# Performance work log

Measured on AMD Instinct MI355X. Metric: run time of the kernel, lower is better.

## Reference

```python
import jax, jax.numpy as jnp
import numpy as np

B, T, M, E, H = 8, 1024, 8192, 1024, 128
DECAY = 0.01
LQ_ADD = 1e-4
POS_TABLE_SIZE = 32


def setup_inputs() -> dict:
    key = jax.random.key(0)
    ks = jax.random.split(key, 9)
    return {
        "block_pos_list": jax.random.randint(ks[0], (B,), 0, 10),
        "inp": jax.random.normal(ks[1], (B, T, E), jnp.float32),
        "memory": jax.random.normal(ks[2], (B, M, E), jnp.float32),
        "memory_block_dist": jax.random.randint(ks[3], (B, M), 0, 1000).astype(jnp.int32),
        "memory_rank": jax.random.normal(ks[4], (B, M), jnp.float32),
        "pos_table": jax.random.normal(ks[5], (POS_TABLE_SIZE, E), jnp.float32) * 0.02,
        "Wk": jax.random.normal(ks[6], (H, E), jnp.float32) / np.float32(np.sqrt(E)),
        "Wq": jax.random.normal(ks[7], (H, E), jnp.float32) / np.float32(np.sqrt(E)),
        "Wv": jax.random.normal(ks[8], (H, E), jnp.float32) / np.float32(np.sqrt(E)),
    }


def reference(block_pos_list, inp, memory, memory_block_dist, memory_rank, pos_table, Wk, Wq, Wv):
    # --- reset slots where block_pos == 0 (start of a new work) ---
    reset = (block_pos_list == 0)                               # [B]
    memory = jnp.where(reset[:, None, None], 0.0, memory)       # [B, M, E]
    dist = jnp.where(reset[:, None], 0, memory_block_dist) + 1  # [B, M]

    # --- log2-bucketed positional embedding added to memory ---
    m_pos_ix = jnp.floor(jnp.log2(dist.astype(jnp.float32))).astype(jnp.int32)
    m_with_emb = memory + pos_table[m_pos_ix]                   # [B, M, E]
    mk = jnp.concatenate([m_with_emb, inp], axis=1)             # [B, M+T, E]

    # --- projections (torch Linear: x @ W.T) ---
    k = jnp.einsum('bse,he->bsh', mk, Wk)                       # [B, M+T, H]
    q = jnp.einsum('bte,he->bth', inp, Wq)                      # [B, T, H]
    v = jnp.einsum('bse,he->bsh', mk, Wv)                       # [B, M+T, H]

    # --- square + max-normalize attention (not softmax) ---
    mbs = M + T
    wei = jnp.einsum('bth,bsh->bts', q, k) * np.float32(mbs ** -0.5)  # [B, T, M+T]
    wei = wei * wei
    wei = wei / jnp.max(wei, axis=2, keepdims=True)

    # --- per-slot rank update ---
    mean_wei = jnp.mean(jnp.sum(wei, axis=1), axis=1)           # [B]
    new_rank = memory_rank + jnp.sum(wei[:, :, :M], axis=1) / mean_wei[:, None] - 1.0 - DECAY

    # --- sort memory slots by rank (descending), evict bottom block ---
    order = jnp.argsort(-new_rank, axis=1)                      # [B, M]
    mem_s = jnp.take_along_axis(memory, order[:, :, None], axis=1)
    dist_s = jnp.take_along_axis(dist, order, axis=1)
    rank_s = jnp.take_along_axis(new_rank, order, axis=1)
    r = min(T, M)
    new_memory = jax.lax.stop_gradient(mem_s.at[:, -r:].set(inp[:, -r:]))
    new_dist = dist_s.at[:, -r:].set(0)
    new_rank_out = jax.lax.stop_gradient(rank_s.at[:, -r:].set(1.0))

    qt_loss = jnp.sum(jnp.log(wei + LQ_ADD))
    out = jnp.einsum('bts,bsh->bth', wei, v)                    # [B, T, H]
    return out, qt_loss, new_memory, new_dist, new_rank_out
```

## Files before the change

kernel.cpp:

```cpp
#include <hip/hip_runtime.h>
#include <hip/hip_bf16.h>
#include <stdint.h>

#define BB 8
#define TT 1024
#define MM 8192
#define EE 1024
#define HH 128
#define SS (MM + TT)
#define RKEEP (MM - 1024)
#define NSPLIT 8
#define SCHUNK (SS / NSPLIT)
#define NT (SCHUNK / 64)
#define BK 32

typedef __attribute__((ext_vector_type(8))) short bf16x8;
typedef __attribute__((ext_vector_type(4))) short s16x4;
typedef __attribute__((ext_vector_type(4))) float f32x4;

#define VMCNT(n) asm volatile("s_waitcnt vmcnt(" #n ")" ::: "memory")
#define LGKM0()  asm volatile("s_waitcnt lgkmcnt(0)" ::: "memory")
#define SBAR()   __builtin_amdgcn_s_barrier()
#define SCB()    __builtin_amdgcn_sched_barrier(0)

static __device__ __forceinline__ unsigned f2ord(float f) {
    unsigned u = __float_as_uint(f);
    return u ^ ((u & 0x80000000u) ? 0xFFFFFFFFu : 0x80000000u);
}
static __device__ __forceinline__ float ord2f(unsigned o) {
    unsigned u = (o & 0x80000000u) ? (o ^ 0x80000000u) : ~o;
    return __uint_as_float(u);
}
static __device__ __forceinline__ unsigned short f2bf(float x) {
    unsigned u = __float_as_uint(x);
    unsigned r = u + 0x7FFFu + ((u >> 16) & 1u);
    return (unsigned short)(r >> 16);
}

static __device__ __forceinline__ void gload_lds16(const short* g, short* l) {
    __builtin_amdgcn_global_load_lds(
        (const __attribute__((address_space(1))) void*)g,
        (__attribute__((address_space(3))) void*)l, 16, 0, 0);
}

__device__ const float SCALEF = (float)(1.0 / 96.0);

__global__ __launch_bounds__(256) void k_wsplit(
    const float* __restrict__ Wk, const float* __restrict__ Wq, const float* __restrict__ Wv,
    short* __restrict__ wk, short* __restrict__ wq, short* __restrict__ wv)
{
    int idx = blockIdx.x * 256 + threadIdx.x;
    int m = idx >> 15;
    int o4 = (idx & 32767) * 4;
    const float* W = m == 0 ? Wk : (m == 1 ? Wq : Wv);
    short* D = m == 0 ? wk : (m == 1 ? wq : wv);
    f32x4 v = *(const f32x4*)&W[o4];
    s16x4 h;
#pragma unroll
    for (int j = 0; j < 4; ++j) h[j] = (short)f2bf(v[j]);
    *(s16x4*)&D[o4] = h;
}

__global__ __launch_bounds__(256, 2) void k_proj_kv(
    const float* __restrict__ memory, const int* __restrict__ mbd,
    const int* __restrict__ bpl, const float* __restrict__ pos_table,
    const float* __restrict__ inp,
    const short* __restrict__ wk, const short* __restrict__ wv,
    short* __restrict__ kb, short* __restrict__ vT)
{
    __shared__ __align__(16) short smA[2][64 * 64];
    __shared__ __align__(16) short smB[3][2][128 * 32];

    const int tid = threadIdx.x;
    const int b   = blockIdx.y;
    const int s0  = blockIdx.x * 64;
    const bool reset = (bpl[b] == 0);
    const int lane = tid & 63, wid = tid >> 6;
    const int wc = wid;
    const int fr = lane & 15, fq = lane >> 4;

    const int arow = tid >> 2;
    const int aq   = tid & 3;
    int pix;
    const float* abase;
    {
        int s = s0 + arow;
        if (s < MM) {
            int d = reset ? 1 : (mbd[b * MM + s] + 1);
            pix = 31 - __clz(d);
            abase = reset ? nullptr : &memory[((size_t)b * MM + s) * EE];
        } else {
            pix = -1;
            abase = &inp[((size_t)b * TT + (s - MM)) * EE];
        }
    }

    f32x4 accK[4][2], accV[4][2];
#pragma unroll
    for (int m = 0; m < 4; ++m)
#pragma unroll
        for (int n = 0; n < 2; ++n) {
            accK[m][n] = (f32x4){0.f, 0.f, 0.f, 0.f};
            accV[m][n] = (f32x4){0.f, 0.f, 0.f, 0.f};
        }

    const int wh   = (tid >> 2);
    const int wk8  = (tid & 3) * 8;
    const int wdst = wid * 512;

    auto STAGEW = [&](int e0, int buf) {
#pragma unroll
        for (int p = 0; p < 2; ++p) {
            int h = p * 64 + wh;
            int ec = wk8 ^ ((h & 3) << 3);
            size_t g = (size_t)h * EE + e0 + ec;
            gload_lds16(&wk[g], &smB[buf][0][p * 2048 + wdst]);
            gload_lds16(&wv[g], &smB[buf][1][p * 2048 + wdst]);
        }
    };
    auto LOADP = [&](int p, f32x4 xa[4]) {
        int e0 = p * 64 + aq * 16;
#pragma unroll
        for (int j = 0; j < 4; ++j) {
            f32x4 v = (f32x4){0.f, 0.f, 0.f, 0.f};
            if (abase) v = *(const f32x4*)&abase[e0 + j * 4];
            if (pix >= 0) {
                f32x4 pt = *(const f32x4*)&pos_table[(size_t)pix * EE + e0 + j * 4];
                v[0] += pt[0]; v[1] += pt[1]; v[2] += pt[2]; v[3] += pt[3];
            }
            xa[j] = v;
        }
    };
    auto STOREP = [&](const f32x4 xa[4], int abuf) {
#pragma unroll
        for (int j = 0; j < 2; ++j) {
            bf16x8 h;
#pragma unroll
            for (int c = 0; c < 4; ++c) {
                h[c]     = (short)f2bf(xa[2 * j][c]);
                h[4 + c] = (short)f2bf(xa[2 * j + 1][c]);
            }
            int g = (aq * 2 + j) ^ (arow & 7);
            *(bf16x8*)&smA[abuf][arow * 64 + g * 8] = h;
        }
    };

    f32x4 xa[4];
    LOADP(0, xa);
    STOREP(xa, 0);
    STAGEW(0, 0);
    STAGEW(BK, 1);
    __syncthreads();
    LOADP(1, xa);

    for (int step = 0; step < 32; ++step) {
        if (step == 31)                        { VMCNT(0); }
        else if ((step & 1) || step == 30)     { VMCNT(4); }
        else                                   { VMCNT(8); }
        SBAR(); SCB();
        if (step <= 29) STAGEW((step + 2) * BK, (step + 2) % 3);

        const int wbuf = step % 3;
        const int pbuf = (step >> 1) & 1;
        bf16x8 ah[4];
#pragma unroll
        for (int m = 0; m < 4; ++m) {
            int r = m * 16 + fr;
            int g = (((step & 1) * 4) + fq) ^ (r & 7);
            ah[m] = *(const bf16x8*)&smA[pbuf][r * 64 + g * 8];
        }
#pragma unroll
        for (int n = 0; n < 2; ++n) {
            int c = wc * 32 + n * 16 + fr;
            int off = c * 32 + ((fq * 8) ^ ((c & 3) << 3));
            bf16x8 kh = *(const bf16x8*)&smB[wbuf][0][off];
            bf16x8 vh = *(const bf16x8*)&smB[wbuf][1][off];
#pragma unroll
            for (int m = 0; m < 4; ++m) {
                accK[m][n] = __builtin_amdgcn_mfma_f32_16x16x32_bf16(ah[m], kh, accK[m][n], 0, 0, 0);
                accV[m][n] = __builtin_amdgcn_mfma_f32_16x16x32_bf16(ah[m], vh, accV[m][n], 0, 0, 0);
            }
        }

        if ((step & 1) && step < 31) {
            STOREP(xa, pbuf ^ 1);
            LGKM0();
            if (step < 29) LOADP((step >> 1) + 2, xa);
        }
    }

#pragma unroll
    for (int m = 0; m < 4; ++m) {
        int row = s0 + m * 16 + fq * 4;
#pragma unroll
        for (int n = 0; n < 2; ++n) {
            int col = wc * 32 + n * 16 + fr;
#pragma unroll
            for (int i = 0; i < 4; ++i)
                kb[((size_t)b * SS + row + i) * HH + col] = (short)f2bf(accK[m][n][i]);
        }
    }
    float* tpT = (float*)smB;
#pragma unroll
    for (int hp = 0; hp < 4; ++hp) {
        __syncthreads();
        if (wc == hp) {
#pragma unroll
            for (int m = 0; m < 4; ++m)
#pragma unroll
                for (int n = 0; n < 2; ++n) {
                    int cl = n * 16 + fr;
                    int row = m * 16 + fq * 4;
                    *(f32x4*)&tpT[cl * 68 + row] = accV[m][n];
                }
        }
        __syncthreads();
        for (int idx = tid; idx < 32 * 16; idx += 256) {
            int hcl = idx >> 4, s4 = (idx & 15) << 2;
            f32x4 v = *(const f32x4*)&tpT[hcl * 68 + s4];
            s16x4 hi;
#pragma unroll
            for (int j = 0; j < 4; ++j) hi[j] = (short)f2bf(v[j]);
            size_t o = ((size_t)b * HH + hp * 32 + hcl) * SS + s0 + s4;
            *(s16x4*)&vT[o] = hi;
        }
    }
}

__global__ __launch_bounds__(256, 4) void k_proj_q(
    const float* __restrict__ inp, const short* __restrict__ wq,
    short* __restrict__ qb)
{
    __shared__ __align__(16) short smA[2][64 * 64];
    __shared__ __align__(16) short smB[3][128 * 32];
    const int tid = threadIdx.x;
    const int b   = blockIdx.y;
    const int t0  = blockIdx.x * 64;
    const int lane = tid & 63, wid = tid >> 6;
    const int wc = wid;
    const int fr = lane & 15, fq = lane >> 4;
    const int arow = tid >> 2, aq = tid & 3;
    const int wh   = (tid >> 2);
    const int wk8  = (tid & 3) * 8;
    const int wdst = wid * 512;
    const float* abase = &inp[((size_t)b * TT + t0 + arow) * EE];

    f32x4 acc[4][2];
#pragma unroll
    for (int m = 0; m < 4; ++m)
#pragma unroll
        for (int n = 0; n < 2; ++n) acc[m][n] = (f32x4){0.f, 0.f, 0.f, 0.f};

    auto STAGEWQ = [&](int e0, int buf) {
#pragma unroll
        for (int p = 0; p < 2; ++p) {
            int h = p * 64 + wh;
            int ec = wk8 ^ ((h & 3) << 3);
            size_t g = (size_t)h * EE + e0 + ec;
            gload_lds16(&wq[g], &smB[buf][p * 2048 + wdst]);
        }
    };
    auto LOADP = [&](int p, f32x4 xa[4]) {
        int e0 = p * 64 + aq * 16;
#pragma unroll
        for (int j = 0; j < 4; ++j) xa[j] = *(const f32x4*)&abase[e0 + j * 4];
    };
    auto STOREP = [&](const f32x4 xa[4], int abuf) {
#pragma unroll
        for (int j = 0; j < 2; ++j) {
            bf16x8 h;
#pragma unroll
            for (int c = 0; c < 4; ++c) {
                h[c]     = (short)f2bf(xa[2 * j][c]);
                h[4 + c] = (short)f2bf(xa[2 * j + 1][c]);
            }
            int g = (aq * 2 + j) ^ (arow & 7);
            *(bf16x8*)&smA[abuf][arow * 64 + g * 8] = h;
        }
    };

    f32x4 xa[4];
    LOADP(0, xa);
    STOREP(xa, 0);
    STAGEWQ(0, 0);
    STAGEWQ(BK, 1);
    __syncthreads();
    LOADP(1, xa);

    for (int step = 0; step < 32; ++step) {
        if (step == 31)                        { VMCNT(0); }
        else if ((step & 1) || step == 30)     { VMCNT(2); }
        else                                   { VMCNT(6); }
        SBAR(); SCB();
        if (step <= 29) STAGEWQ((step + 2) * BK, (step + 2) % 3);

        const int wbuf = step % 3;
        const int pbuf = (step >> 1) & 1;
        bf16x8 ah[4];
#pragma unroll
        for (int m = 0; m < 4; ++m) {
            int r = m * 16 + fr;
            int g = (((step & 1) * 4) + fq) ^ (r & 7);
            ah[m] = *(const bf16x8*)&smA[pbuf][r * 64 + g * 8];
        }
#pragma unroll
        for (int n = 0; n < 2; ++n) {
            int c = wc * 32 + n * 16 + fr;
            int off = c * 32 + ((fq * 8) ^ ((c & 3) << 3));
            bf16x8 bh = *(const bf16x8*)&smB[wbuf][off];
#pragma unroll
            for (int m = 0; m < 4; ++m)
                acc[m][n] = __builtin_amdgcn_mfma_f32_16x16x32_bf16(ah[m], bh, acc[m][n], 0, 0, 0);
        }

        if ((step & 1) && step < 31) {
            STOREP(xa, pbuf ^ 1);
            LGKM0();
            if (step < 29) LOADP((step >> 1) + 2, xa);
        }
    }
#pragma unroll
    for (int m = 0; m < 4; ++m) {
        int row = t0 + m * 16 + fq * 4;
#pragma unroll
        for (int n = 0; n < 2; ++n) {
            int col = wc * 32 + n * 16 + fr;
#pragma unroll
            for (int i = 0; i < 4; ++i)
                qb[((size_t)b * TT + row + i) * HH + col] = (short)f2bf(acc[m][n][i]);
        }
    }
}

__device__ __forceinline__ void stage_k64_async(const short* __restrict__ src,
                                                size_t rowBase, int tid, short* sh)
{
#pragma unroll
    for (int c2 = 0; c2 < 4; ++c2) {
        int srow = c2 * 16 + (tid >> 4);
        int scol = ((tid & 15) * 8) ^ ((srow & 7) << 3);
        size_t g = (rowBase + srow) * HH + scol;
        gload_lds16(&src[g], &sh[c2 * 2048 + (tid >> 6) * 512]);
    }
}

__device__ __forceinline__ void stage_v64_async(const short* __restrict__ vT,
                                                int b, int st, int tid, short* vs)
{
#pragma unroll
    for (int c2 = 0; c2 < 4; ++c2) {
        int h = c2 * 32 + (tid >> 3);
        int sc = ((tid & 7) * 8) ^ ((h & 7) << 3);
        size_t g = ((size_t)b * HH + h) * SS + st + sc;
        gload_lds16(&vT[g], &vs[c2 * 2048 + (tid >> 6) * 512]);
    }
}

__device__ __forceinline__ void load_qfrags(const short* __restrict__ qb,
                                            size_t rowIx, int fq, bf16x8 qh[4])
{
    size_t base = rowIx * HH + fq * 8;
#pragma unroll
    for (int k = 0; k < 4; ++k)
        qh[k] = *(const bf16x8*)&qb[base + k * 32];
}

__device__ __forceinline__ void qk_mfma4(const bf16x8 qh[4], const short* sh,
                                         int fr, int fq, f32x4 acc[4])
{
#pragma unroll
    for (int n = 0; n < 4; ++n) {
        int sc = n * 16 + fr;
        int ro = sc * 128, msk = (sc & 7) << 3;
#pragma unroll
        for (int k = 0; k < 4; ++k) {
            int off = ro + ((k * 32 + fq * 8) ^ msk);
            bf16x8 bh = *(const bf16x8*)&sh[off];
            acc[n] = __builtin_amdgcn_mfma_f32_16x16x32_bf16(qh[k], bh, acc[n], 0, 0, 0);
        }
    }
}

__global__ __launch_bounds__(256) void k_rowmax(
    const short* __restrict__ qb, const short* __restrict__ kb,
    float* __restrict__ rowmax)
{
    __shared__ short Ks[2][64 * 128];
    const int tid = threadIdx.x, lane = tid & 63, wloc = tid >> 6;
    const int fr = lane & 15, fq = lane >> 4;
    const int split = blockIdx.x, t0 = blockIdx.y * 64, b = blockIdx.z;

    bf16x8 qh[4];
    load_qfrags(qb, (size_t)b * TT + t0 + wloc * 16 + fr, fq, qh);

    float rm[4] = {0.f, 0.f, 0.f, 0.f};
    const int sBeg = split * SCHUNK;
    const size_t kbase = (size_t)b * SS;

    stage_k64_async(kb, kbase + sBeg, tid, Ks[0]);
    __syncthreads();
    for (int t = 0; t < NT; ++t) {
        const int bf = t & 1;
        if (t + 1 < NT)
            stage_k64_async(kb, kbase + sBeg + (t + 1) * 64, tid, Ks[bf ^ 1]);
        f32x4 acc[4];
#pragma unroll
        for (int n = 0; n < 4; ++n) acc[n] = (f32x4){0.f, 0.f, 0.f, 0.f};
        qk_mfma4(qh, Ks[bf], fr, fq, acc);
#pragma unroll
        for (int n = 0; n < 4; ++n)
#pragma unroll
            for (int i = 0; i < 4; ++i) {
                float w = acc[n][i] * SCALEF;
                rm[i] = fmaxf(rm[i], w * w);
            }
        __syncthreads();
    }
#pragma unroll
    for (int d = 1; d < 16; d <<= 1)
#pragma unroll
        for (int i = 0; i < 4; ++i)
            rm[i] = fmaxf(rm[i], __shfl_xor(rm[i], d, 64));
    if (fr == 0)
#pragma unroll
        for (int i = 0; i < 4; ++i)
            atomicMax((int*)&rowmax[b * TT + t0 + wloc * 16 + fq * 4 + i], __float_as_int(rm[i]));
}

__global__ __launch_bounds__(256) void k_attn(
    const short* __restrict__ qb, const short* __restrict__ kb,
    const short* __restrict__ vT,
    const float* __restrict__ rowmax,
    float* __restrict__ outAcc, float* __restrict__ cpart, float* __restrict__ qtloss)
{
    __shared__ short Ks[2][64 * 128];
    __shared__ short Vs[2][128 * 64];
    __shared__ short Ph[64 * 64];
    __shared__ float csLDS[SCHUNK];
    __shared__ float qred[256];
    const int tid = threadIdx.x, lane = tid & 63, wloc = tid >> 6;
    const int fr = lane & 15, fq = lane >> 4;
    const int split = blockIdx.x, t0 = blockIdx.y * 64, b = blockIdx.z;

    for (int i = tid; i < SCHUNK; i += 256) csLDS[i] = 0.f;

    bf16x8 qh[4];
    load_qfrags(qb, (size_t)b * TT + t0 + wloc * 16 + fr, fq, qh);

    float inv[4];
#pragma unroll
    for (int i = 0; i < 4; ++i)
        inv[i] = 1.0f / rowmax[b * TT + t0 + wloc * 16 + fq * 4 + i];

    f32x4 oacc[8];
#pragma unroll
    for (int n = 0; n < 8; ++n) oacc[n] = (f32x4){0.f, 0.f, 0.f, 0.f};
    float qtp = 0.f;

    const int sBeg = split * SCHUNK;
    const size_t kbase = (size_t)b * SS;

    stage_k64_async(kb, kbase + sBeg, tid, Ks[0]);
    stage_v64_async(vT, b, sBeg, tid, Vs[0]);

    for (int t = 0; t < NT; ++t) {
        const int bf = t & 1;
        __syncthreads();

        if (t + 1 < NT) {
            stage_k64_async(kb, kbase + sBeg + (t + 1) * 64, tid, Ks[bf ^ 1]);
            stage_v64_async(vT, b, sBeg + (t + 1) * 64, tid, Vs[bf ^ 1]);
        }

        f32x4 acc[4];
#pragma unroll
        for (int n = 0; n < 4; ++n) acc[n] = (f32x4){0.f, 0.f, 0.f, 0.f};
        qk_mfma4(qh, Ks[bf], fr, fq, acc);

#pragma unroll
        for (int n = 0; n < 4; ++n) {
            float cp = 0.f;
#pragma unroll
            for (int i = 0; i < 4; ++i) {
                float w = acc[n][i] * SCALEF;
                float w2 = w * w;
                float wei = w2 * inv[i];
                qtp += __logf(wei + 1e-4f);
                cp += wei;
                int r = wloc * 16 + fq * 4 + i;
                int sw = (n * 16 + fr) ^ ((r & 7) << 3);
                Ph[r * 64 + sw] = (short)f2bf(wei);
            }
            cp += __shfl_xor(cp, 16, 64);
            cp += __shfl_xor(cp, 32, 64);
            if (fq == 0) atomicAdd(&csLDS[t * 64 + n * 16 + fr], cp);
        }
        LGKM0(); SBAR(); SCB();
        {
            int rA = wloc * 16 + fr;
#pragma unroll
            for (int k = 0; k < 2; ++k) {
                int offA = rA * 64 + ((k * 32 + fq * 8) ^ ((rA & 7) << 3));
                bf16x8 ph = *(const bf16x8*)&Ph[offA];
#pragma unroll
                for (int n = 0; n < 8; ++n) {
                    int hc = n * 16 + fr;
                    int offB = hc * 64 + ((k * 32 + fq * 8) ^ ((hc & 7) << 3));
                    bf16x8 vh = *(const bf16x8*)&Vs[bf][offB];
                    oacc[n] = __builtin_amdgcn_mfma_f32_16x16x32_bf16(ph, vh, oacc[n], 0, 0, 0);
                }
            }
        }
    }

#pragma unroll
    for (int n = 0; n < 8; ++n)
#pragma unroll
        for (int i = 0; i < 4; ++i)
            atomicAdd(&outAcc[((size_t)b * TT + t0 + wloc * 16 + fq * 4 + i) * HH + n * 16 + fr],
                      oacc[n][i]);

    qred[tid] = qtp;
    __syncthreads();
    for (int off = 128; off; off >>= 1) {
        if (tid < off) qred[tid] += qred[tid + off];
        __syncthreads();
    }
    if (tid == 0) atomicAdd(qtloss, qred[0]);

    const int tt = blockIdx.y;
    for (int s = tid; s < SCHUNK; s += 256)
        cpart[((size_t)(b * 16 + tt)) * SS + sBeg + s] = csLDS[s];
}

__global__ __launch_bounds__(256) void k_rank(
    const float* __restrict__ cpart, const float* __restrict__ mrank,
    unsigned long long* __restrict__ keys, float* __restrict__ csum)
{
    const int b = blockIdx.x, tid = threadIdx.x;
    __shared__ float red[256];
    float p = 0.f;
    for (int s = tid; s < SS; s += 256) {
        float cs = 0.f;
#pragma unroll
        for (int tt = 0; tt < 16; ++tt) cs += cpart[((size_t)(b * 16 + tt)) * SS + s];
        csum[b * SS + s] = cs;
        p += cs;
    }
    red[tid] = p;
    __syncthreads();
    for (int off = 128; off; off >>= 1) {
        if (tid < off) red[tid] += red[tid + off];
        __syncthreads();
    }
    float mean = red[0] / (float)SS;
    for (int m = tid; m < MM; m += 256) {
        float rank = ((mrank[b * MM + m] + csum[b * SS + m] / mean) - 1.0f) - 0.01f;
        keys[b * MM + m] = ((unsigned long long)(unsigned)(~f2ord(rank)) << 32) | (unsigned)m;
    }
}

__global__ __launch_bounds__(1024) void k_sort(unsigned long long* __restrict__ keys)
{
    __shared__ unsigned long long a[MM];
    const int b = blockIdx.x, tid = threadIdx.x;
    for (int i = tid; i < MM; i += 1024) a[i] = keys[(size_t)b * MM + i];
    __syncthreads();
    for (int k = 2; k <= MM; k <<= 1) {
        for (int j = k >> 1; j > 0; j >>= 1) {
            for (int i = tid; i < MM; i += 1024) {
                int l = i ^ j;
                if (l > i) {
                    unsigned long long x = a[i], y = a[l];
                    bool up = ((i & k) == 0);
                    if ((x > y) == up) { a[i] = y; a[l] = x; }
                }
            }
            __syncthreads();
        }
    }
    for (int i = tid; i < MM; i += 1024) keys[(size_t)b * MM + i] = a[i];
}

__global__ __launch_bounds__(256) void k_scatter(
    const float* __restrict__ memory, const int* __restrict__ mbd,
    const int* __restrict__ bpl, const float* __restrict__ inp,
    const unsigned long long* __restrict__ keys,
    float* __restrict__ nmem, float* __restrict__ ndist, float* __restrict__ nrank)
{
    const int blk = blockIdx.x;
    const int b = blk >> 10;
    const int p0 = (blk & 1023) * 8;
    const bool reset = (bpl[b] == 0);
    const int tid = threadIdx.x;
    const f32x4 zero = (f32x4){0.f, 0.f, 0.f, 0.f};

    f32x4 vr[8];
    float dist[8], rankv[8];
#pragma unroll
    for (int r = 0; r < 8; ++r) {
        int p = p0 + r;
        if (p < RKEEP) {
            unsigned long long key = keys[(size_t)b * MM + p];
            int src = (int)(unsigned)(key & 0xFFFFFFFFu);
            vr[r] = reset ? zero
                          : *(const f32x4*)&memory[((size_t)b * MM + src) * EE + tid * 4];
            dist[r]  = reset ? 1.0f : (float)(mbd[b * MM + src] + 1);
            rankv[r] = ord2f(~(unsigned)(key >> 32));
        } else {
            int irow = p - RKEEP;
            vr[r] = *(const f32x4*)&inp[((size_t)b * TT + irow) * EE + tid * 4];
            dist[r] = 0.f; rankv[r] = 1.0f;
        }
    }
#pragma unroll
    for (int r = 0; r < 8; ++r) {
        int p = p0 + r;
        *(f32x4*)&nmem[((size_t)b * MM + p) * EE + tid * 4] = vr[r];
        if (tid == 0) { ndist[b * MM + p] = dist[r]; nrank[b * MM + p] = rankv[r]; }
    }
}

extern "C" void kernel_launch(void* const* d_in, const int* in_sizes, int n_in,
                              void* d_out, int out_size, void* d_ws, size_t ws_size,
                              hipStream_t stream)
{
    const int*   bpl    = (const int*)d_in[0];
    const float* inp    = (const float*)d_in[1];
    const float* memory = (const float*)d_in[2];
    const int*   mbd    = (const int*)d_in[3];
    const float* mrank  = (const float*)d_in[4];
    const float* pos    = (const float*)d_in[5];
    const float* Wk     = (const float*)d_in[6];
    const float* Wq     = (const float*)d_in[7];
    const float* Wv     = (const float*)d_in[8];

    float* out   = (float*)d_out;
    float* qtl   = out + (size_t)BB * TT * HH;
    float* nmem  = qtl + 1;
    float* ndist = nmem + (size_t)BB * MM * EE;
    float* nrank = ndist + (size_t)BB * MM;

    char* w = (char*)d_ws;
    short* qb = (short*)w; w += (size_t)BB * TT * HH * 2;
    short* kb = (short*)w; w += (size_t)BB * SS * HH * 2;
    short* vT = (short*)w; w += (size_t)BB * HH * SS * 2;
    float* rmax = (float*)w; w += (size_t)BB * TT * 4;
    float* csum = (float*)w; w += (size_t)BB * SS * 4;
    float* cpart = (float*)w; w += (size_t)BB * 16 * SS * 4;
    unsigned long long* keys = (unsigned long long*)w; w += (size_t)BB * MM * 8;
    short* wk = (short*)w; w += (size_t)HH * EE * 2;
    short* wq = (short*)w; w += (size_t)HH * EE * 2;
    short* wv = (short*)w; w += (size_t)HH * EE * 2;
    if ((size_t)(w - (char*)d_ws) > ws_size) return;

    hipMemsetAsync(d_out, 0, ((size_t)BB * TT * HH + 1) * 4, stream);
    hipMemsetAsync(rmax, 0, (size_t)BB * TT * 4, stream);

    k_wsplit <<<384, 256, 0, stream>>>(Wk, Wq, Wv, wk, wq, wv);
    k_proj_kv<<<dim3(SS / 64, BB), 256, 0, stream>>>(memory, mbd, bpl, pos, inp,
                                                     wk, wv, kb, vT);
    k_proj_q <<<dim3(TT / 64, BB), 256, 0, stream>>>(inp, wq, qb);
    k_rowmax <<<dim3(NSPLIT, TT / 64, BB), 256, 0, stream>>>(qb, kb, rmax);
    k_attn   <<<dim3(NSPLIT, TT / 64, BB), 256, 0, stream>>>(qb, kb, vT,
                                                             rmax, out, cpart, qtl);
    k_rank   <<<BB, 256, 0, stream>>>(cpart, mrank, keys, csum);
    k_sort   <<<BB, 1024, 0, stream>>>(keys);
    k_scatter<<<BB * (MM / 8), 256, 0, stream>>>(memory, mbd, bpl, inp, keys, nmem, ndist, nrank);
}
```

Before: 597.4 us.

## Precompute bf16 memory+pos and input matrix, stage projections via async LDS loads

Adds a pre-pass kernel that builds the concatenated memory-plus-positional-embedding and input matrix in bf16 in the workspace. The K/V and Q projection kernels then stage both operands directly into LDS with async global-to-LDS loads in a triple-buffered pipeline, replacing register-side fp32 loading and conversion. This simplifies the projection pipelines and removes conversion work from their inner loops. The cost is an extra pass that writes and re-reads a large bf16 intermediate, adding substantial global memory traffic.

```diff
diff --git a/kernel.cpp b/kernel.cpp
--- a/kernel.cpp
+++ b/kernel.cpp
@@ -19,7 +19,6 @@
 typedef __attribute__((ext_vector_type(4))) float f32x4;
 
 #define VMCNT(n) asm volatile("s_waitcnt vmcnt(" #n ")" ::: "memory")
-#define LGKM0()  asm volatile("s_waitcnt lgkmcnt(0)" ::: "memory")
 #define SBAR()   __builtin_amdgcn_s_barrier()
 #define SCB()    __builtin_amdgcn_sched_barrier(0)
 
@@ -61,39 +60,73 @@
     *(s16x4*)&D[o4] = h;
 }
 
-__global__ __launch_bounds__(256, 2) void k_proj_kv(
+__global__ __launch_bounds__(256) void k_mkprep(
     const float* __restrict__ memory, const int* __restrict__ mbd,
     const int* __restrict__ bpl, const float* __restrict__ pos_table,
-    const float* __restrict__ inp,
+    const float* __restrict__ inp, short* __restrict__ mkb)
+{
+    const int blk = blockIdx.x;
+    const int b = blk / 144, chunk = blk % 144;
+    const bool reset = (bpl[b] == 0);
+    const int tid = threadIdx.x;
+    const int e4 = tid * 4;
+    for (int i = 0; i < 64; ++i) {
+        int s = chunk * 64 + i;
+        f32x4 v;
+        if (s < MM) {
+            int d = reset ? 1 : (mbd[b * MM + s] + 1);
+            int pix = 31 - __clz(d);
+            f32x4 pt = *(const f32x4*)&pos_table[(size_t)pix * EE + e4];
+            if (reset) {
+                v = pt;
+            } else {
+                f32x4 mv = *(const f32x4*)&memory[((size_t)b * MM + s) * EE + e4];
+                v[0] = mv[0] + pt[0]; v[1] = mv[1] + pt[1];
+                v[2] = mv[2] + pt[2]; v[3] = mv[3] + pt[3];
+            }
+        } else {
+            v = *(const f32x4*)&inp[((size_t)b * TT + (s - MM)) * EE + e4];
+        }
+        s16x4 h;
+#pragma unroll
+        for (int j = 0; j < 4; ++j) h[j] = (short)f2bf(v[j]);
+        *(s16x4*)&mkb[((size_t)b * SS + s) * EE + e4] = h;
+    }
+}
+
+__device__ __forceinline__ void stage_a32(const short* __restrict__ src,
+                                          size_t rowBase, int e0, int tid, short* sa)
+{
+    int r = tid >> 2, g = tid & 3;
+    int scol = (g ^ ((r >> 1) & 3)) << 3;
+    gload_lds16(&src[rowBase + (size_t)r * EE + e0 + scol], &sa[(tid >> 6) * 512]);
+}
+__device__ __forceinline__ void stage_w32(const short* __restrict__ src,
+                                          int e0, int tid, short* sw)
+{
+#pragma unroll
+    for (int c2 = 0; c2 < 2; ++c2) {
+        int h = c2 * 64 + (tid >> 2), g = tid & 3;
+        int scol = (g ^ ((h >> 1) & 3)) << 3;
+        gload_lds16(&src[(size_t)h * EE + e0 + scol], &sw[c2 * 2048 + (tid >> 6) * 512]);
+    }
+}
+
+__global__ __launch_bounds__(256, 2) void k_proj_kv(
+    const short* __restrict__ mkb,
     const short* __restrict__ wk, const short* __restrict__ wv,
     short* __restrict__ kb, short* __restrict__ vT)
 {
-    __shared__ __align__(16) short smA[2][64 * 64];
+    __shared__ __align__(16) short smA[3][64 * 32];
     __shared__ __align__(16) short smB[3][2][128 * 32];
 
     const int tid = threadIdx.x;
     const int b   = blockIdx.y;
     const int s0  = blockIdx.x * 64;
-    const bool reset = (bpl[b] == 0);
     const int lane = tid & 63, wid = tid >> 6;
     const int wc = wid;
     const int fr = lane & 15, fq = lane >> 4;
-
-    const int arow = tid >> 2;
-    const int aq   = tid & 3;
-    int pix;
-    const float* abase;
-    {
-        int s = s0 + arow;
-        if (s < MM) {
-            int d = reset ? 1 : (mbd[b * MM + s] + 1);
-            pix = 31 - __clz(d);
-            abase = reset ? nullptr : &memory[((size_t)b * MM + s) * EE];
-        } else {
-            pix = -1;
-            abase = &inp[((size_t)b * TT + (s - MM)) * EE];
-        }
-    }
+    const size_t arowBase = ((size_t)b * SS + s0) * EE;
 
     f32x4 accK[4][2], accV[4][2];
 #pragma unroll
@@ -104,88 +137,38 @@
             accV[m][n] = (f32x4){0.f, 0.f, 0.f, 0.f};
         }
 
-    const int wh   = (tid >> 2);
-    const int wk8  = (tid & 3) * 8;
-    const int wdst = wid * 512;
-
-    auto STAGEW = [&](int e0, int buf) {
-#pragma unroll
-        for (int p = 0; p < 2; ++p) {
-            int h = p * 64 + wh;
-            int ec = wk8 ^ ((h & 3) << 3);
-            size_t g = (size_t)h * EE + e0 + ec;
-            gload_lds16(&wk[g], &smB[buf][0][p * 2048 + wdst]);
-            gload_lds16(&wv[g], &smB[buf][1][p * 2048 + wdst]);
-        }
+    auto STAGE = [&](int step, int buf) {
+        stage_a32(mkb, arowBase, step * BK, tid, smA[buf]);
+        stage_w32(wk, step * BK, tid, smB[buf][0]);
+        stage_w32(wv, step * BK, tid, smB[buf][1]);
     };
-    auto LOADP = [&](int p, f32x4 xa[4]) {
-        int e0 = p * 64 + aq * 16;
-#pragma unroll
-        for (int j = 0; j < 4; ++j) {
-            f32x4 v = (f32x4){0.f, 0.f, 0.f, 0.f};
-            if (abase) v = *(const f32x4*)&abase[e0 + j * 4];
-            if (pix >= 0) {
-                f32x4 pt = *(const f32x4*)&pos_table[(size_t)pix * EE + e0 + j * 4];
-                v[0] += pt[0]; v[1] += pt[1]; v[2] += pt[2]; v[3] += pt[3];
-            }
-            xa[j] = v;
-        }
-    };
-    auto STOREP = [&](const f32x4 xa[4], int abuf) {
-#pragma unroll
-        for (int j = 0; j < 2; ++j) {
-            bf16x8 h;
-#pragma unroll
-            for (int c = 0; c < 4; ++c) {
-                h[c]     = (short)f2bf(xa[2 * j][c]);
-                h[4 + c] = (short)f2bf(xa[2 * j + 1][c]);
-            }
-            int g = (aq * 2 + j) ^ (arow & 7);
-            *(bf16x8*)&smA[abuf][arow * 64 + g * 8] = h;
-        }
-    };
-
-    f32x4 xa[4];
-    LOADP(0, xa);
-    STOREP(xa, 0);
-    STAGEW(0, 0);
-    STAGEW(BK, 1);
-    __syncthreads();
-    LOADP(1, xa);
+
+    STAGE(0, 0);
+    STAGE(1, 1);
 
     for (int step = 0; step < 32; ++step) {
-        if (step == 31)                        { VMCNT(0); }
-        else if ((step & 1) || step == 30)     { VMCNT(4); }
-        else                                   { VMCNT(8); }
+        if (step == 31) { VMCNT(0); } else { VMCNT(5); }
         SBAR(); SCB();
-        if (step <= 29) STAGEW((step + 2) * BK, (step + 2) % 3);
-
-        const int wbuf = step % 3;
-        const int pbuf = (step >> 1) & 1;
+        if (step <= 29) STAGE(step + 2, (step + 2) % 3);
+
+        const int buf = step % 3;
         bf16x8 ah[4];
 #pragma unroll
         for (int m = 0; m < 4; ++m) {
             int r = m * 16 + fr;
-            int g = (((step & 1) * 4) + fq) ^ (r & 7);
-            ah[m] = *(const bf16x8*)&smA[pbuf][r * 64 + g * 8];
+            ah[m] = *(const bf16x8*)&smA[buf][r * 32 + ((fq ^ ((r >> 1) & 3)) << 3)];
         }
 #pragma unroll
         for (int n = 0; n < 2; ++n) {
             int c = wc * 32 + n * 16 + fr;
-            int off = c * 32 + ((fq * 8) ^ ((c & 3) << 3));
-            bf16x8 kh = *(const bf16x8*)&smB[wbuf][0][off];
-            bf16x8 vh = *(const bf16x8*)&smB[wbuf][1][off];
+            int off = c * 32 + ((fq ^ ((c >> 1) & 3)) << 3);
+            bf16x8 kh = *(const bf16x8*)&smB[buf][0][off];
+            bf16x8 vh = *(const bf16x8*)&smB[buf][1][off];
 #pragma unroll
             for (int m = 0; m < 4; ++m) {
                 accK[m][n] = __builtin_amdgcn_mfma_f32_16x16x32_bf16(ah[m], kh, accK[m][n], 0, 0, 0);
                 accV[m][n] = __builtin_amdgcn_mfma_f32_16x16x32_bf16(ah[m], vh, accV[m][n], 0, 0, 0);
             }
-        }
-
-        if ((step & 1) && step < 31) {
-            STOREP(xa, pbuf ^ 1);
-            LGKM0();
-            if (step < 29) LOADP((step >> 1) + 2, xa);
         }
     }
 
@@ -227,11 +210,11 @@
     }
 }
 
-__global__ __launch_bounds__(256, 4) void k_proj_q(
-    const float* __restrict__ inp, const short* __restrict__ wq,
+__global__ __launch_bounds__(256) void k_proj_q(
+    const short* __restrict__ mkb, const short* __restrict__ wq,
     short* __restrict__ qb)
 {
-    __shared__ __align__(16) short smA[2][64 * 64];
+    __shared__ __align__(16) short smA[3][64 * 32];
     __shared__ __align__(16) short smB[3][128 * 32];
     const int tid = threadIdx.x;
     const int b   = blockIdx.y;
@@ -239,11 +222,7 @@
     const int lane = tid & 63, wid = tid >> 6;
     const int wc = wid;
     const int fr = lane & 15, fq = lane >> 4;
-    const int arow = tid >> 2, aq = tid & 3;
-    const int wh   = (tid >> 2);
-    const int wk8  = (tid & 3) * 8;
-    const int wdst = wid * 512;
-    const float* abase = &inp[((size_t)b * TT + t0 + arow) * EE];
+    const size_t arowBase = ((size_t)b * SS + MM + t0) * EE;
 
     f32x4 acc[4][2];
 #pragma unroll
@@ -251,72 +230,34 @@
 #pragma unroll
         for (int n = 0; n < 2; ++n) acc[m][n] = (f32x4){0.f, 0.f, 0.f, 0.f};
 
-    auto STAGEWQ = [&](int e0, int buf) {
-#pragma unroll
-        for (int p = 0; p < 2; ++p) {
-            int h = p * 64 + wh;
-            int ec = wk8 ^ ((h & 3) << 3);
-            size_t g = (size_t)h * EE + e0 + ec;
-            gload_lds16(&wq[g], &smB[buf][p * 2048 + wdst]);
-        }
+    auto STAGE = [&](int step, int buf) {
+        stage_a32(mkb, arowBase, step * BK, tid, smA[buf]);
+        stage_w32(wq, step * BK, tid, smB[buf]);
     };
-    auto LOADP = [&](int p, f32x4 xa[4]) {
-        int e0 = p * 64 + aq * 16;
-#pragma unroll
-        for (int j = 0; j < 4; ++j) xa[j] = *(const f32x4*)&abase[e0 + j * 4];
-    };
-    auto STOREP = [&](const f32x4 xa[4], int abuf) {
-#pragma unroll
-        for (int j = 0; j < 2; ++j) {
-            bf16x8 h;
-#pragma unroll
-            for (int c = 0; c < 4; ++c) {
-                h[c]     = (short)f2bf(xa[2 * j][c]);
-                h[4 + c] = (short)f2bf(xa[2 * j + 1][c]);
-            }
-            int g = (aq * 2 + j) ^ (arow & 7);
-            *(bf16x8*)&smA[abuf][arow * 64 + g * 8] = h;
-        }
-    };
-
-    f32x4 xa[4];
-    LOADP(0, xa);
-    STOREP(xa, 0);
-    STAGEWQ(0, 0);
-    STAGEWQ(BK, 1);
-    __syncthreads();
-    LOADP(1, xa);
+
+    STAGE(0, 0);
+    STAGE(1, 1);
 
     for (int step = 0; step < 32; ++step) {
-        if (step == 31)                        { VMCNT(0); }
-        else if ((step & 1) || step == 30)     { VMCNT(2); }
-        else                                   { VMCNT(6); }
+        if (step == 31) { VMCNT(0); } else { VMCNT(3); }
         SBAR(); SCB();
-        if (step <= 29) STAGEWQ((step + 2) * BK, (step + 2) % 3);
-
-        const int wbuf = step % 3;
-        const int pbuf = (step >> 1) & 1;
+        if (step <= 29) STAGE(step + 2, (step + 2) % 3);
+
+        const int buf = step % 3;
         bf16x8 ah[4];
 #pragma unroll
         for (int m = 0; m < 4; ++m) {
             int r = m * 16 + fr;
-            int g = (((step & 1) * 4) + fq) ^ (r & 7);
-            ah[m] = *(const bf16x8*)&smA[pbuf][r * 64 + g * 8];
+            ah[m] = *(const bf16x8*)&smA[buf][r * 32 + ((fq ^ ((r >> 1) & 3)) << 3)];
         }
 #pragma unroll
         for (int n = 0; n < 2; ++n) {
             int c = wc * 32 + n * 16 + fr;
-            int off = c * 32 + ((fq * 8) ^ ((c & 3) << 3));
-            bf16x8 bh = *(const bf16x8*)&smB[wbuf][off];
+            int off = c * 32 + ((fq ^ ((c >> 1) & 3)) << 3);
+            bf16x8 bh = *(const bf16x8*)&smB[buf][off];
 #pragma unroll
             for (int m = 0; m < 4; ++m)
                 acc[m][n] = __builtin_amdgcn_mfma_f32_16x16x32_bf16(ah[m], bh, acc[m][n], 0, 0, 0);
-        }
-
-        if ((step & 1) && step < 31) {
-            STOREP(xa, pbuf ^ 1);
-            LGKM0();
-            if (step < 29) LOADP((step >> 1) + 2, xa);
         }
     }
 #pragma unroll
@@ -495,7 +436,8 @@
             cp += __shfl_xor(cp, 32, 64);
             if (fq == 0) atomicAdd(&csLDS[t * 64 + n * 16 + fr], cp);
         }
-        LGKM0(); SBAR(); SCB();
+        asm volatile("s_waitcnt lgkmcnt(0)" ::: "memory");
+        SBAR(); SCB();
         {
             int rA = wloc * 16 + fr;
 #pragma unroll
@@ -652,15 +594,16 @@
     short* wk = (short*)w; w += (size_t)HH * EE * 2;
     short* wq = (short*)w; w += (size_t)HH * EE * 2;
     short* wv = (short*)w; w += (size_t)HH * EE * 2;
+    short* mkb = (short*)w; w += (size_t)BB * SS * EE * 2;
     if ((size_t)(w - (char*)d_ws) > ws_size) return;
 
     hipMemsetAsync(d_out, 0, ((size_t)BB * TT * HH + 1) * 4, stream);
     hipMemsetAsync(rmax, 0, (size_t)BB * TT * 4, stream);
 
     k_wsplit <<<384, 256, 0, stream>>>(Wk, Wq, Wv, wk, wq, wv);
-    k_proj_kv<<<dim3(SS / 64, BB), 256, 0, stream>>>(memory, mbd, bpl, pos, inp,
-                                                     wk, wv, kb, vT);
-    k_proj_q <<<dim3(TT / 64, BB), 256, 0, stream>>>(inp, wq, qb);
+    k_mkprep <<<BB * 144, 256, 0, stream>>>(memory, mbd, bpl, pos, inp, mkb);
+    k_proj_kv<<<dim3(SS / 64, BB), 256, 0, stream>>>(mkb, wk, wv, kb, vT);
+    k_proj_q <<<dim3(TT / 64, BB), 256, 0, stream>>>(mkb, wq, qb);
     k_rowmax <<<dim3(NSPLIT, TT / 64, BB), 256, 0, stream>>>(qb, kb, rmax);
     k_attn   <<<dim3(NSPLIT, TT / 64, BB), 256, 0, stream>>>(qb, kb, vT,
                                                              rmax, out, cpart, qtl);
```

Measured after the change: 649.2 us. 1.09x slower.
